# Optimization experiments

Hardware: AMD Instinct MI355X
Metric: run time of the kernel (lower is better)

## Reference

```python
import jax, jax.numpy as jnp
import numpy as np

L, B, T, C, H, V, CTX = 4, 2, 1024, 1024, 16, 50257, 2048
D = C // H
EPS = 1e-5
NEG_SLOPE = 0.01


def layer_norm(x, w, b):
    mu = jnp.mean(x, axis=-1, keepdims=True)
    var = jnp.mean(jnp.square(x - mu), axis=-1, keepdims=True)
    return (x - mu) * jax.lax.rsqrt(var + EPS) * w + b


def setup_inputs() -> dict:
    key = jax.random.key(0)
    ks = jax.random.split(key, 8)
    s = 0.02  # init std as in _init_weights
    return {
        "idx": jax.random.randint(ks[0], (B, T), 0, V),
        "wte": jax.random.normal(ks[1], (V, C), jnp.float32) * s,
        "wpe": jax.random.normal(ks[2], (CTX, C), jnp.float32) * s,
        "ln1_w": jnp.ones((L, C), jnp.float32),
        "ln1_b": jnp.zeros((L, C), jnp.float32),
        "attn_w": jax.random.normal(ks[3], (L, C, 3 * C), jnp.float32) * s,
        "attn_b": jnp.zeros((L, 3 * C), jnp.float32),
        "proj_w": jax.random.normal(ks[4], (L, C, C), jnp.float32) * s,
        "proj_b": jnp.zeros((L, C), jnp.float32),
        "ln2_w": jnp.ones((L, C), jnp.float32),
        "ln2_b": jnp.zeros((L, C), jnp.float32),
        "fc_w": jax.random.normal(ks[5], (L, C, 4 * C), jnp.float32) * s,
        "fc_b": jnp.zeros((L, 4 * C), jnp.float32),
        "fcproj_w": jax.random.normal(ks[6], (L, 4 * C, C), jnp.float32) * s,
        "fcproj_b": jnp.zeros((L, C), jnp.float32),
        "lnf_w": jnp.ones((C,), jnp.float32),
        "lnf_b": jnp.zeros((C,), jnp.float32),
    }


def reference(idx, wte, wpe, ln1_w, ln1_b, attn_w, attn_b, proj_w, proj_b,
              ln2_w, ln2_b, fc_w, fc_b, fcproj_w, fcproj_b, lnf_w, lnf_b):
    t = idx.shape[1]
    x = wte[idx] + wpe[:t]  # [B,T,C]; dropout=0 => identity
    causal = jnp.tril(jnp.ones((t, t), bool))  # [T,T]
    scale = 1.0 / np.sqrt(D)
    for l in range(L):
        # --- causal self-attention ---
        h = layer_norm(x, ln1_w[l], ln1_b[l])
        qkv = h @ attn_w[l] + attn_b[l]  # [B,T,3C]
        q, k, v = jnp.split(qkv, 3, axis=-1)
        q = q.reshape(B, t, H, D)
        k = k.reshape(B, t, H, D)
        v = v.reshape(B, t, H, D)
        att = jnp.einsum('bthd,bshd->bhts', q, k) * scale  # [B,H,T,T]
        att = jnp.where(causal, att, -jnp.inf)
        att = jax.nn.softmax(att, axis=-1)
        y = jnp.einsum('bhts,bshd->bthd', att, v).reshape(B, t, C)
        x = x + y @ proj_w[l] + proj_b[l]
        # --- MLP ---
        h = layer_norm(x, ln2_w[l], ln2_b[l])
        h = h @ fc_w[l] + fc_b[l]
        h = jnp.where(h >= 0, h, NEG_SLOPE * h)  # LeakyReLU(0.01)
        x = x + h @ fcproj_w[l] + fcproj_b[l]
    x = layer_norm(x, lnf_w, lnf_b)
    # targets=None path: lm_head on last position only, tied weight = wte
    logits = x[:, -1:, :] @ wte.T  # [B,1,V]
    return logits
```

## Files before the change

### kernel.cpp

```cpp
#include <hip/hip_runtime.h>
#include <hip/hip_bf16.h>


#define TT 1024
#define CC 1024
#define NHEAD 16
#define DHEAD 64
#define NBATCH 2
#define VOCAB 50257

typedef __attribute__((ext_vector_type(8))) short bf16x8;
typedef __attribute__((ext_vector_type(4))) float f32x4;

#define GPTR(p) (const __attribute__((address_space(1))) void*)(p)
#define LPTR(p) (__attribute__((address_space(3))) void*)(p)

__device__ __forceinline__ unsigned short f2bf(float f) {
  union { float f; unsigned u; } v; v.f = f;
  unsigned r = v.u + 0x7fffu + ((v.u >> 16) & 1u);
  return (unsigned short)(r >> 16);
}
__device__ __forceinline__ float bf2f(unsigned short u) {
  union { unsigned u; float f; } v; v.u = ((unsigned)u) << 16;
  return v.f;
}

__device__ __forceinline__ f32x4 mfma_bf16(bf16x8 a, bf16x8 b, f32x4 c) {
  return __builtin_amdgcn_mfma_f32_16x16x32_bf16(a, b, c, 0, 0, 0);
}

__device__ __forceinline__ unsigned pk2(float lo, float hi) {
  return (unsigned)f2bf(lo) | ((unsigned)f2bf(hi) << 16);
}

__global__ __launch_bounds__(256) void embedln_k(const int* __restrict__ idx,
    const float* __restrict__ wte, const float* __restrict__ wpe,
    const float* __restrict__ lw, const float* __restrict__ lb,
    float* __restrict__ x, unsigned short* __restrict__ h)
{
  __shared__ float rs[4], rss[4];
  const int row = blockIdx.x;
  const int t = row & (TT - 1);
  const int tok = idx[row];
  const int tid = threadIdx.x, wave = tid >> 6, lane = tid & 63;
  float4 va = ((const float4*)(wte + (size_t)tok * CC))[tid];
  float4 vp = ((const float4*)(wpe + (size_t)t * CC))[tid];
  float4 v = make_float4(va.x + vp.x, va.y + vp.y, va.z + vp.z, va.w + vp.w);
  ((float4*)(x + (size_t)row * CC))[tid] = v;
  float s  = v.x + v.y + v.z + v.w;
  float ss = v.x*v.x + v.y*v.y + v.z*v.z + v.w*v.w;
#pragma unroll
  for (int off = 1; off < 64; off <<= 1) {
    s  += __shfl_xor(s, off, 64);
    ss += __shfl_xor(ss, off, 64);
  }
  if (lane == 0) { rs[wave] = s; rss[wave] = ss; }
  __syncthreads();
  s  = rs[0] + rs[1] + rs[2] + rs[3];
  ss = rss[0] + rss[1] + rss[2] + rss[3];
  float mu = s * (1.f / CC);
  float var = ss * (1.f / CC) - mu * mu;
  float rstd = rsqrtf(var + 1e-5f);
  float4 wv = ((const float4*)lw)[tid];
  float4 bv = ((const float4*)lb)[tid];
  float o0 = (v.x - mu) * rstd * wv.x + bv.x;
  float o1 = (v.y - mu) * rstd * wv.y + bv.y;
  float o2 = (v.z - mu) * rstd * wv.z + bv.z;
  float o3 = (v.w - mu) * rstd * wv.w + bv.w;
  ((uint2*)(h + (size_t)row * CC))[tid] = make_uint2(pk2(o0, o1), pk2(o2, o3));
}

__global__ __launch_bounds__(256) void redln_k(float* __restrict__ x,
    const float* __restrict__ P, const float* __restrict__ bias,
    const float* __restrict__ lw, const float* __restrict__ lb,
    unsigned short* __restrict__ out, int splits)
{
  int row = blockIdx.x * 4 + (threadIdx.x >> 6);
  int lane = threadIdx.x & 63;
  const int c0 = lane * 16;
  float* xw = x + (size_t)row * CC + c0;
  float4 v[4];
#pragma unroll
  for (int i = 0; i < 4; ++i) v[i] = *(const float4*)(xw + i * 4);
  {
    const float4* b4 = (const float4*)(bias + c0);
#pragma unroll
    for (int i = 0; i < 4; ++i) {
      float4 bv = b4[i];
      v[i].x += bv.x; v[i].y += bv.y; v[i].z += bv.z; v[i].w += bv.w;
    }
  }
  for (int sp = 0; sp < splits; ++sp) {
    const float4* p4 = (const float4*)(P + ((size_t)sp * 2048 + row) * CC + c0);
#pragma unroll
    for (int i = 0; i < 4; ++i) {
      float4 pv = p4[i];
      v[i].x += pv.x; v[i].y += pv.y; v[i].z += pv.z; v[i].w += pv.w;
    }
  }
  float s = 0.f, ss = 0.f;
#pragma unroll
  for (int i = 0; i < 4; ++i) {
    *(float4*)(xw + i * 4) = v[i];
    s  += v[i].x + v[i].y + v[i].z + v[i].w;
    ss += v[i].x*v[i].x + v[i].y*v[i].y + v[i].z*v[i].z + v[i].w*v[i].w;
  }
#pragma unroll
  for (int off = 1; off < 64; off <<= 1) {
    s  += __shfl_xor(s, off, 64);
    ss += __shfl_xor(ss, off, 64);
  }
  float mu = s * (1.f / CC);
  float var = ss * (1.f / CC) - mu * mu;
  float rstd = rsqrtf(var + 1e-5f);
  const float* wr = lw + c0;
  const float* br = lb + c0;
  unsigned q[8];
#pragma unroll
  for (int i = 0; i < 4; ++i) {
    float4 wv = *(const float4*)(wr + i * 4);
    float4 bv = *(const float4*)(br + i * 4);
    float o0 = (v[i].x - mu) * rstd * wv.x + bv.x;
    float o1 = (v[i].y - mu) * rstd * wv.y + bv.y;
    float o2 = (v[i].z - mu) * rstd * wv.z + bv.z;
    float o3 = (v[i].w - mu) * rstd * wv.w + bv.w;
    q[i*2+0] = pk2(o0, o1);
    q[i*2+1] = pk2(o2, o3);
  }
  uint4* op = (uint4*)(out + (size_t)row * CC + c0);
  op[0] = make_uint4(q[0], q[1], q[2], q[3]);
  op[1] = make_uint4(q[4], q[5], q[6], q[7]);
}

__global__ __launch_bounds__(256) void wconv_all_k(
    const float* __restrict__ attn_w, unsigned short* __restrict__ wt_attn,
    const float* __restrict__ proj_w, unsigned short* __restrict__ wt_proj,
    const float* __restrict__ fc_w,   unsigned short* __restrict__ wt_fc,
    const float* __restrict__ fcp_w,  unsigned short* __restrict__ wt_fcp)
{
  int b = blockIdx.x;
  const float* W; unsigned short* Wt; int K, N, kx, ny;
  if (b < 3072) {
    int layer = b / 768, tI = b % 768;
    K = 1024; N = 3072;
    W = attn_w + (size_t)layer * K * N; Wt = wt_attn + (size_t)layer * K * N;
    kx = tI % 16; ny = tI / 16;
  } else if (b < 3840) {
    b -= 3072; int layer = b / 256, tI = b % 256;
    K = 1024; N = 1024;
    W = proj_w + (size_t)layer * K * N; Wt = wt_proj + (size_t)layer * K * N;
    kx = tI % 16; ny = tI / 16;
  } else if (b < 6912) {
    b -= 3840; int layer = b / 1024, tI = b % 1024;
    K = 1024; N = 4096;
    W = fc_w + (size_t)layer * K * N; Wt = wt_fc + (size_t)layer * K * N;
    kx = tI % 16; ny = tI / 16;
  } else {
    b -= 6912; int layer = b / 1024, tI = b % 1024;
    K = 4096; N = 1024;
    W = fcp_w + (size_t)layer * K * N; Wt = wt_fcp + (size_t)layer * K * N;
    kx = tI % 64; ny = tI / 64;
  }
  __shared__ float tile[64][65];
  const int k0 = kx << 6, n0 = ny << 6;
  const int t = threadIdx.x;
  {
    const int r = t >> 4, c4 = t & 15;
#pragma unroll
    for (int p = 0; p < 4; ++p) {
      int kr = r + (p << 4);
      float4 v = *(const float4*)(W + (size_t)(k0 + kr) * N + n0 + (c4 << 2));
      tile[kr][(c4 << 2) + 0] = v.x;
      tile[kr][(c4 << 2) + 1] = v.y;
      tile[kr][(c4 << 2) + 2] = v.z;
      tile[kr][(c4 << 2) + 3] = v.w;
    }
  }
  __syncthreads();
  {
    const int n = t >> 2, kq = t & 3;
    bf16x8 o0, o1;
#pragma unroll
    for (int e = 0; e < 8; ++e) o0[e] = (short)f2bf(tile[(kq << 4) + e][n]);
#pragma unroll
    for (int e = 0; e < 8; ++e) o1[e] = (short)f2bf(tile[(kq << 4) + 8 + e][n]);
    unsigned short* dst = Wt + (size_t)(n0 + n) * K + k0 + (kq << 4);
    *(bf16x8*)dst = o0;
    *(bf16x8*)(dst + 8) = o1;
  }
}

#define MODE_QKV  0
#define MODE_PART 1
#define MODE_FC   2

template<int MODE>
__global__ __launch_bounds__(256) void gemm_k(
    const unsigned short* __restrict__ A,
    const unsigned short* __restrict__ Wt,
    const float* __restrict__ bias,
    float* __restrict__ pbuf,
    unsigned short* __restrict__ obf,
    unsigned short* __restrict__ q_o,
    unsigned short* __restrict__ k_o,
    unsigned short* __restrict__ v_o,
    int M, int N, int K, int kchunk, int ncol0)
{
  __shared__ alignas(16) unsigned short Asm[2][128 * 64];
  __shared__ alignas(16) unsigned short Bsm[2][128 * 64];
  const int tid  = threadIdx.x;
  const int wave = tid >> 6, lane = tid & 63;
  const int lg = lane >> 4, ll = lane & 15;
  const int nTM = M >> 7, nTN = N >> 7;
  int bid = blockIdx.x;
  const int mt = bid % nTM; bid /= nTM;
  const int nt = bid % nTN;
  const int s  = bid / nTN;
  const int m0 = mt << 7, n0 = nt << 7;
  const int kb = s * kchunk;
  const int nIter = kchunk >> 6;
  const int wm = (wave >> 1) << 6, wn = (wave & 1) << 6;
  f32x4 acc[4][4] = {};

#define STAGE(BUF, K0)                                                        \
  {                                                                           \
    _Pragma("unroll")                                                         \
    for (int c = 0; c < 4; ++c) {                                             \
      const int seg = (wave << 2) + c;                                        \
      const int g = (seg << 6) + lane;                                        \
      const int row = g >> 3, kq = g & 7;                                     \
      const unsigned short* asrc = A  + (size_t)(m0 + row) * K + (K0) + (kq << 3); \
      const unsigned short* bsrc = Wt + (size_t)(n0 + row) * K + (K0) + (kq << 3); \
      __builtin_amdgcn_global_load_lds(GPTR(asrc), LPTR(&Asm[BUF][seg << 9]), 16, 0, 0); \
      __builtin_amdgcn_global_load_lds(GPTR(bsrc), LPTR(&Bsm[BUF][seg << 9]), 16, 0, 0); \
    }                                                                         \
  }

  STAGE(0, kb);
  if (nIter > 1) STAGE(1, kb + 64);

  for (int t = 0; t < nIter; ++t) {
    const int cur = t & 1;
    if (t + 1 < nIter) { asm volatile("s_waitcnt vmcnt(8)" ::: "memory"); }
    else               { asm volatile("s_waitcnt vmcnt(0)" ::: "memory"); }
    __builtin_amdgcn_sched_barrier(0);
    __builtin_amdgcn_s_barrier();

    const unsigned short* As = &Asm[cur][0];
    const unsigned short* Bs = &Bsm[cur][0];
#pragma unroll
    for (int kk = 0; kk < 2; ++kk) {
      bf16x8 af[4], bfr[4];
#pragma unroll
      for (int i = 0; i < 4; ++i)
        af[i] = *(const bf16x8*)(As + ((wm + i * 16 + ll) << 6) + (kk << 5) + (lg << 3));
#pragma unroll
      for (int j = 0; j < 4; ++j)
        bfr[j] = *(const bf16x8*)(Bs + ((wn + j * 16 + ll) << 6) + (kk << 5) + (lg << 3));
#pragma unroll
      for (int i = 0; i < 4; ++i)
#pragma unroll
        for (int j = 0; j < 4; ++j)
          acc[i][j] = mfma_bf16(af[i], bfr[j], acc[i][j]);
    }
    __builtin_amdgcn_sched_barrier(0);
    __builtin_amdgcn_s_barrier();
    if (t + 2 < nIter) STAGE(cur, kb + ((t + 2) << 6));
  }
#undef STAGE

#pragma unroll
  for (int j = 0; j < 4; ++j) {
    int gc = n0 + wn + j * 16 + ll;
    int gcol = ncol0 + gc;
    float bv = (MODE == MODE_PART) ? 0.f : bias[gcol];
#pragma unroll
    for (int i = 0; i < 4; ++i) {
      int gr0 = m0 + wm + i * 16 + (lg << 2);
#pragma unroll
      for (int r = 0; r < 4; ++r) {
        int grow = gr0 + r;
        float val = acc[i][j][r] + bv;
        if (MODE == MODE_QKV) {
          int which = gcol >> 10;
          int head = (gcol >> 6) & 15;
          int d = gcol & 63;
          int bb = grow >> 10, tt2 = grow & (TT - 1);
          unsigned short* dst = (which == 0) ? q_o : (which == 1) ? k_o : v_o;
          dst[(((size_t)((bb << 4) + head)) << 16) + ((size_t)tt2 << 6) + d] = f2bf(val);
        } else if (MODE == MODE_FC) {
          val = (val >= 0.f) ? val : 0.01f * val;
          obf[(size_t)grow * N + gc] = f2bf(val);
        } else {
          pbuf[((size_t)s * M + grow) * N + gc] = val;
        }
      }
    }
  }
}

__global__ __launch_bounds__(256) void attn_k(
    const unsigned short* __restrict__ Qb,
    const unsigned short* __restrict__ Kb,
    const unsigned short* __restrict__ Vb,
    unsigned short* __restrict__ ybuf)
{
  __shared__ alignas(16) unsigned short Ksm[64][72];
  __shared__ alignas(16) unsigned short Vtsm[64][64];
  __shared__ alignas(16) unsigned short Psm[4][16][72];
  const int tid = threadIdx.x;
  const int wave = tid >> 6, lane = tid & 63;
  const int lg = lane >> 4, ll = lane & 15;
  const int qt = blockIdx.x & 15, bh = blockIdx.x >> 4;
  const int b = bh >> 4, h = bh & 15;
  const size_t base = (size_t)bh << 16;
  const int q0 = qt << 6;
  const float SC = 0.125f * 1.44269504f;

  const int qrow = q0 + wave * 16 + ll;
  bf16x8 aq0 = *(const bf16x8*)(Qb + base + ((size_t)qrow << 6) + (lg << 3));
  bf16x8 aq1 = *(const bf16x8*)(Qb + base + ((size_t)qrow << 6) + 32 + (lg << 3));

  f32x4 accy[4] = {};
  float m_run[4], l_run[4];
#pragma unroll
  for (int r = 0; r < 4; ++r) { m_run[r] = -1e30f; l_run[r] = 0.f; }

  const int sk_row = tid >> 3, sk_cq = tid & 7;
  const int sv_d = tid & 63, sv_kq = tid >> 6;
  const int qg0 = q0 + wave * 16 + (lg << 2);

  for (int kb = 0; kb <= qt; ++kb) {
    const int kbase = kb << 6;
#pragma unroll
    for (int p = 0; p < 2; ++p) {
      int r = sk_row + (p << 5);
      bf16x8 kv = *(const bf16x8*)(Kb + base + ((size_t)(kbase + r) << 6) + (sk_cq << 3));
      *(bf16x8*)&Ksm[r][sk_cq << 3] = kv;
    }
#pragma unroll
    for (int p = 0; p < 2; ++p) {
      int kq8 = sv_kq + (p << 2);
      bf16x8 wv;
#pragma unroll
      for (int e = 0; e < 8; ++e)
        wv[e] = (short)Vb[base + ((size_t)(kbase + (kq8 << 3) + e) << 6) + sv_d];
      int u = kq8 ^ (sv_d & 7);
      *(bf16x8*)&Vtsm[sv_d][u << 3] = wv;
    }
    __syncthreads();

    float p_[4][4];
    float rmax[4] = {-1e30f, -1e30f, -1e30f, -1e30f};
#pragma unroll
    for (int kk = 0; kk < 4; ++kk) {
      f32x4 z = {};
      bf16x8 bk0 = *(const bf16x8*)&Ksm[kk * 16 + ll][lg << 3];
      bf16x8 bk1 = *(const bf16x8*)&Ksm[kk * 16 + ll][32 + (lg << 3)];
      z = mfma_bf16(aq0, bk0, z);
      z = mfma_bf16(aq1, bk1, z);
      int key = kbase + kk * 16 + ll;
#pragma unroll
      for (int r = 0; r < 4; ++r) {
        float v = z[r] * SC;
        v = (key > qg0 + r) ? -1e30f : v;
        p_[kk][r] = v;
        rmax[r] = fmaxf(rmax[r], v);
      }
    }
#pragma unroll
    for (int off = 1; off < 16; off <<= 1)
#pragma unroll
      for (int r = 0; r < 4; ++r)
        rmax[r] = fmaxf(rmax[r], __shfl_xor(rmax[r], off, 64));

    float alpha[4], rsum[4];
#pragma unroll
    for (int r = 0; r < 4; ++r) {
      float mn = fmaxf(m_run[r], rmax[r]);
      alpha[r] = exp2f(m_run[r] - mn);
      m_run[r] = mn;
      rsum[r] = 0.f;
    }
#pragma unroll
    for (int kk = 0; kk < 4; ++kk)
#pragma unroll
      for (int r = 0; r < 4; ++r) {
        float e = exp2f(p_[kk][r] - m_run[r]);
        p_[kk][r] = e;
        rsum[r] += e;
      }
#pragma unroll
    for (int off = 1; off < 16; off <<= 1)
#pragma unroll
      for (int r = 0; r < 4; ++r)
        rsum[r] += __shfl_xor(rsum[r], off, 64);
#pragma unroll
    for (int r = 0; r < 4; ++r)
      l_run[r] = l_run[r] * alpha[r] + rsum[r];
#pragma unroll
    for (int df = 0; df < 4; ++df)
#pragma unroll
      for (int r = 0; r < 4; ++r)
        accy[df][r] *= alpha[r];

#pragma unroll
    for (int kk = 0; kk < 4; ++kk)
#pragma unroll
      for (int r = 0; r < 4; ++r)
        Psm[wave][(lg << 2) + r][kk * 16 + ll] = f2bf(p_[kk][r]);
    bf16x8 pa0 = *(const bf16x8*)&Psm[wave][ll][lg << 3];
    bf16x8 pa1 = *(const bf16x8*)&Psm[wave][ll][32 + (lg << 3)];

#pragma unroll
    for (int df = 0; df < 4; ++df) {
      int d = df * 16 + ll;
      int u0 = lg ^ (d & 7);
      int u1 = (4 + lg) ^ (d & 7);
      bf16x8 bv0 = *(const bf16x8*)&Vtsm[d][u0 << 3];
      bf16x8 bv1 = *(const bf16x8*)&Vtsm[d][u1 << 3];
      accy[df] = mfma_bf16(pa0, bv0, accy[df]);
      accy[df] = mfma_bf16(pa1, bv1, accy[df]);
    }
    __syncthreads();
  }

#pragma unroll
  for (int df = 0; df < 4; ++df)
#pragma unroll
    for (int r = 0; r < 4; ++r) {
      int qr = qg0 + r;
      float y = accy[df][r] / l_run[r];
      ybuf[(((size_t)((b << 10) + qr)) << 10) + (h << 6) + df * 16 + ll] = f2bf(y);
    }
}


__global__ __launch_bounds__(256) void qlast_k(
    const unsigned short* __restrict__ hbuf,
    const float* __restrict__ Wq,
    float* __restrict__ qpart)
{
  __shared__ float xs[2][128];
  const int tid = threadIdx.x, ks = blockIdx.y;
  {
    const int b = tid >> 7, j = tid & 127;
    xs[b][j] = bf2f(hbuf[((size_t)(b * TT + TT - 1)) * CC + ks * 128 + j]);
  }
  __syncthreads();
  const int n = blockIdx.x * 256 + tid;
  float a0 = 0.f, a1 = 0.f;
  const float* wp = Wq + (size_t)(ks * 128) * 3072 + n;
  for (int k = 0; k < 128; k += 8)
#pragma unroll
    for (int u = 0; u < 8; ++u) {
      float w = wp[(size_t)(k + u) * 3072];
      a0 += xs[0][k + u] * w;
      a1 += xs[1][k + u] * w;
    }
  qpart[(size_t)(ks * 2 + 0) * 1024 + n] = a0;
  qpart[(size_t)(ks * 2 + 1) * 1024 + n] = a1;
}

__global__ __launch_bounds__(256) void attnlast2_k(
    const float* __restrict__ qpart, const float* __restrict__ bq,
    const unsigned short* __restrict__ Kb,
    const unsigned short* __restrict__ Vb,
    float* __restrict__ y_last)
{
  __shared__ float qs[64];
  __shared__ float wm[4], wl[4], wacc[4][64];
  const int tid = threadIdx.x;
  const int wave = tid >> 6, lane = tid & 63;
  const int bh = blockIdx.x;
  const int b = bh >> 4, h = bh & 15;
  const size_t base = (size_t)bh << 16;
  if (tid < 64) {
    const int col = h * 64 + tid;
    float q = bq[col];
#pragma unroll
    for (int ks = 0; ks < 8; ++ks)
      q += qpart[(size_t)(ks * 2 + b) * 1024 + col];
    qs[tid] = q;
  }
  __syncthreads();

  float m_w = -1e30f, l_w = 0.f, acc = 0.f;
  for (int ks = 0; ks < 4; ++ks) {
    const int key = ks * 256 + wave * 64 + lane;
    float s = 0.f;
    const unsigned short* kp = Kb + base + ((size_t)key << 6);
#pragma unroll
    for (int o = 0; o < 8; ++o) {
      bf16x8 kv = *(const bf16x8*)(kp + (o << 3));
#pragma unroll
      for (int e = 0; e < 8; ++e)
        s += qs[(o << 3) + e] * bf2f((unsigned short)kv[e]);
    }
    s *= 0.125f;
    float m = s;
#pragma unroll
    for (int off = 1; off < 64; off <<= 1)
      m = fmaxf(m, __shfl_xor(m, off, 64));
    float mn = fmaxf(m_w, m);
    float alpha = __expf(m_w - mn);
    m_w = mn;
    float p = __expf(s - mn);
    float ps = p;
#pragma unroll
    for (int off = 1; off < 64; off <<= 1)
      ps += __shfl_xor(ps, off, 64);
    l_w = l_w * alpha + ps;
    float a2 = 0.f;
    const unsigned short* vp = Vb + base + ((size_t)(ks * 256 + wave * 64) << 6);
    for (int j = 0; j < 64; ++j) {
      float pj = __shfl(p, j, 64);
      a2 += pj * bf2f(vp[((size_t)j << 6) + lane]);
    }
    acc = acc * alpha + a2;
  }
  if (lane == 0) { wm[wave] = m_w; wl[wave] = l_w; }
  wacc[wave][lane] = acc;
  __syncthreads();
  if (wave == 0) {
    float m0 = fmaxf(fmaxf(wm[0], wm[1]), fmaxf(wm[2], wm[3]));
    float lt = 0.f, at = 0.f;
#pragma unroll
    for (int sI = 0; sI < 4; ++sI) {
      float f = __expf(wm[sI] - m0);
      lt += wl[sI] * f;
      at += wacc[sI][lane] * f;
    }
    y_last[b * CC + h * 64 + lane] = at / lt;
  }
}

__global__ __launch_bounds__(256) void projpart_k(
    const float* __restrict__ ylast,
    const float* __restrict__ W,
    float* __restrict__ ppart)
{
  __shared__ float xs[2][128];
  const int tid = threadIdx.x, ks = blockIdx.y;
  {
    const int b = tid >> 7, j = tid & 127;
    xs[b][j] = ylast[b * 1024 + ks * 128 + j];
  }
  __syncthreads();
  const int n = blockIdx.x * 256 + tid;
  float a0 = 0.f, a1 = 0.f;
  const float* wp = W + (size_t)(ks * 128) * 1024 + n;
  for (int k = 0; k < 128; k += 8)
#pragma unroll
    for (int u = 0; u < 8; ++u) {
      float w = wp[(size_t)(k + u) * 1024];
      a0 += xs[0][k + u] * w;
      a1 += xs[1][k + u] * w;
    }
  ppart[(size_t)(ks * 2 + 0) * 1024 + n] = a0;
  ppart[(size_t)(ks * 2 + 1) * 1024 + n] = a1;
}

__global__ __launch_bounds__(256) void fclast_k(
    const float* __restrict__ x, const float* __restrict__ ppart,
    const float* __restrict__ pbias,
    const float* __restrict__ lw, const float* __restrict__ lb,
    const float* __restrict__ W,
    float* __restrict__ fcpart)
{
  __shared__ float xs[2][1024];
  const int tid = threadIdx.x;
  const int wave = tid >> 6, lane = tid & 63;
  if (wave < 2) {
    const int c0 = lane * 16;
    const float* xr = x + ((size_t)(wave * TT + TT - 1)) * CC + c0;
    float4 v[4];
    float s = 0.f, ss = 0.f;
#pragma unroll
    for (int i = 0; i < 4; ++i) {
      v[i] = *(const float4*)(xr + i * 4);
      float4 bv = *(const float4*)(pbias + c0 + i * 4);
      v[i].x += bv.x; v[i].y += bv.y; v[i].z += bv.z; v[i].w += bv.w;
    }
#pragma unroll
    for (int sp = 0; sp < 8; ++sp) {
      const float* pp = ppart + (size_t)(sp * 2 + wave) * 1024 + c0;
#pragma unroll
      for (int i = 0; i < 4; ++i) {
        float4 pv = *(const float4*)(pp + i * 4);
        v[i].x += pv.x; v[i].y += pv.y; v[i].z += pv.z; v[i].w += pv.w;
      }
    }
#pragma unroll
    for (int i = 0; i < 4; ++i) {
      s  += v[i].x + v[i].y + v[i].z + v[i].w;
      ss += v[i].x*v[i].x + v[i].y*v[i].y + v[i].z*v[i].z + v[i].w*v[i].w;
    }
#pragma unroll
    for (int off = 1; off < 64; off <<= 1) {
      s  += __shfl_xor(s, off, 64);
      ss += __shfl_xor(ss, off, 64);
    }
    float mu = s * (1.f / CC);
    float var = ss * (1.f / CC) - mu * mu;
    float rstd = rsqrtf(var + 1e-5f);
#pragma unroll
    for (int i = 0; i < 4; ++i) {
      float4 wv = *(const float4*)(lw + c0 + i * 4);
      float4 bv = *(const float4*)(lb + c0 + i * 4);
      xs[wave][c0 + i * 4 + 0] = (v[i].x - mu) * rstd * wv.x + bv.x;
      xs[wave][c0 + i * 4 + 1] = (v[i].y - mu) * rstd * wv.y + bv.y;
      xs[wave][c0 + i * 4 + 2] = (v[i].z - mu) * rstd * wv.z + bv.z;
      xs[wave][c0 + i * 4 + 3] = (v[i].w - mu) * rstd * wv.w + bv.w;
    }
  }
  __syncthreads();
  const int ks = blockIdx.y;
  const int n = blockIdx.x * 256 + tid;
  float a0 = 0.f, a1 = 0.f;
  const float* wp = W + (size_t)(ks * 128) * 4096 + n;
  for (int k = 0; k < 128; k += 8)
#pragma unroll
    for (int u = 0; u < 8; ++u) {
      float w = wp[(size_t)(k + u) * 4096];
      a0 += xs[0][ks * 128 + k + u] * w;
      a1 += xs[1][ks * 128 + k + u] * w;
    }
  fcpart[(size_t)(ks * 2 + 0) * 4096 + n] = a0;
  fcpart[(size_t)(ks * 2 + 1) * 4096 + n] = a1;
}

__global__ __launch_bounds__(256) void fcprojpart_k(
    const float* __restrict__ fcpart, const float* __restrict__ fcbias,
    const float* __restrict__ W,
    float* __restrict__ fppart)
{
  __shared__ float hs[2][512];
  const int tid = threadIdx.x, ks = blockIdx.y;
#pragma unroll
  for (int i = 0; i < 4; ++i) {
    const int e = tid + 256 * i;
    const int b = e >> 9, j = e & 511;
    const int c = ks * 512 + j;
    float v = fcbias[c];
#pragma unroll
    for (int sp = 0; sp < 8; ++sp)
      v += fcpart[(size_t)(sp * 2 + b) * 4096 + c];
    hs[b][j] = (v >= 0.f) ? v : 0.01f * v;
  }
  __syncthreads();
  const int n = blockIdx.x * 256 + tid;
  float a0 = 0.f, a1 = 0.f;
  const float* wp = W + (size_t)(ks * 512) * 1024 + n;
  for (int k = 0; k < 512; k += 8)
#pragma unroll
    for (int u = 0; u < 8; ++u) {
      float w = wp[(size_t)(k + u) * 1024];
      a0 += hs[0][k + u] * w;
      a1 += hs[1][k + u] * w;
    }
  fppart[(size_t)(ks * 2 + 0) * 1024 + n] = a0;
  fppart[(size_t)(ks * 2 + 1) * 1024 + n] = a1;
}

__global__ void lnfmerge_k(const float* __restrict__ x,
    const float* __restrict__ ppart, const float* __restrict__ pbias,
    const float* __restrict__ fppart, const float* __restrict__ fpbias,
    const float* __restrict__ lw, const float* __restrict__ lb,
    float* __restrict__ xf)
{
  const int row = blockIdx.x;
  const int lane = threadIdx.x;
  const int c0 = lane * 16;
  const float* xr = x + ((size_t)(row * TT + TT - 1)) * CC + c0;
  float4 v[4];
  float s = 0.f, ss = 0.f;
#pragma unroll
  for (int i = 0; i < 4; ++i) {
    v[i] = *(const float4*)(xr + i * 4);
    float4 b1 = *(const float4*)(pbias + c0 + i * 4);
    float4 b2 = *(const float4*)(fpbias + c0 + i * 4);
    v[i].x += b1.x + b2.x; v[i].y += b1.y + b2.y;
    v[i].z += b1.z + b2.z; v[i].w += b1.w + b2.w;
  }
#pragma unroll
  for (int sp = 0; sp < 8; ++sp) {
    const float* p1 = ppart + (size_t)(sp * 2 + row) * 1024 + c0;
    const float* p2 = fppart + (size_t)(sp * 2 + row) * 1024 + c0;
#pragma unroll
    for (int i = 0; i < 4; ++i) {
      float4 a = *(const float4*)(p1 + i * 4);
      float4 b = *(const float4*)(p2 + i * 4);
      v[i].x += a.x + b.x; v[i].y += a.y + b.y;
      v[i].z += a.z + b.z; v[i].w += a.w + b.w;
    }
  }
#pragma unroll
  for (int i = 0; i < 4; ++i) {
    s  += v[i].x + v[i].y + v[i].z + v[i].w;
    ss += v[i].x*v[i].x + v[i].y*v[i].y + v[i].z*v[i].z + v[i].w*v[i].w;
  }
#pragma unroll
  for (int off = 1; off < 64; off <<= 1) {
    s  += __shfl_xor(s, off, 64);
    ss += __shfl_xor(ss, off, 64);
  }
  float mu = s * (1.f / CC);
  float var = ss * (1.f / CC) - mu * mu;
  float rstd = rsqrtf(var + 1e-5f);
  float* op = xf + (size_t)row * CC + c0;
#pragma unroll
  for (int i = 0; i < 4; ++i) {
    float4 wv = *(const float4*)(lw + c0 + i * 4);
    float4 bv = *(const float4*)(lb + c0 + i * 4);
    float4 o;
    o.x = (v[i].x - mu) * rstd * wv.x + bv.x;
    o.y = (v[i].y - mu) * rstd * wv.y + bv.y;
    o.z = (v[i].z - mu) * rstd * wv.z + bv.z;
    o.w = (v[i].w - mu) * rstd * wv.w + bv.w;
    *(float4*)(op + i * 4) = o;
  }
}

__global__ __launch_bounds__(256) void head_k(const float* __restrict__ xf,
    const float* __restrict__ wte, float* __restrict__ out)
{
  int v = (blockIdx.x << 2) + (threadIdx.x >> 6);
  if (v >= VOCAB) return;
  int lane = threadIdx.x & 63;
  const float4* wr = (const float4*)(wte + (size_t)v * CC);
  const float4* x0 = (const float4*)xf;
  const float4* x1 = (const float4*)(xf + CC);
  float a0 = 0.f, a1 = 0.f;
#pragma unroll
  for (int i = 0; i < 4; ++i) {
    float4 wv = wr[lane + i * 64];
    float4 p0 = x0[lane + i * 64];
    float4 p1 = x1[lane + i * 64];
    a0 += wv.x * p0.x + wv.y * p0.y + wv.z * p0.z + wv.w * p0.w;
    a1 += wv.x * p1.x + wv.y * p1.y + wv.z * p1.z + wv.w * p1.w;
  }
#pragma unroll
  for (int off = 1; off < 64; off <<= 1) {
    a0 += __shfl_xor(a0, off, 64);
    a1 += __shfl_xor(a1, off, 64);
  }
  if (lane == 0) {
    out[v] = a0;
    out[VOCAB + v] = a1;
  }
}

extern "C" void kernel_launch(void* const* d_in, const int* in_sizes, int n_in,
                              void* d_out, int out_size, void* d_ws, size_t ws_size,
                              hipStream_t stream)
{
  const int*   idx      = (const int*)d_in[0];
  const float* wte      = (const float*)d_in[1];
  const float* wpe      = (const float*)d_in[2];
  const float* ln1_w    = (const float*)d_in[3];
  const float* ln1_b    = (const float*)d_in[4];
  const float* attn_w   = (const float*)d_in[5];
  const float* attn_b   = (const float*)d_in[6];
  const float* proj_w   = (const float*)d_in[7];
  const float* proj_b   = (const float*)d_in[8];
  const float* ln2_w    = (const float*)d_in[9];
  const float* ln2_b    = (const float*)d_in[10];
  const float* fc_w     = (const float*)d_in[11];
  const float* fc_b     = (const float*)d_in[12];
  const float* fcproj_w = (const float*)d_in[13];
  const float* fcproj_b = (const float*)d_in[14];
  const float* lnf_w    = (const float*)d_in[15];
  const float* lnf_b    = (const float*)d_in[16];
  float* out = (float*)d_out;

  const size_t MB = 1u << 20;
  char* ws = (char*)d_ws;
  float*          x   = (float*)ws;
  unsigned short* h   = (unsigned short*)(ws + 8*MB);
  unsigned short* qb  = (unsigned short*)(ws + 12*MB);
  unsigned short* kb_ = (unsigned short*)(ws + 16*MB);
  unsigned short* vb  = (unsigned short*)(ws + 20*MB);
  unsigned short* yb  = (unsigned short*)(ws + 24*MB);
  unsigned short* hf  = (unsigned short*)(ws + 28*MB);
  char* sm = ws + 44*MB;
  float* xf     = (float*)(sm + 0);
  float* ylast  = (float*)(sm + 16*1024);
  float* qpart  = (float*)(sm + 64*1024);
  float* ppart  = (float*)(sm + 128*1024);
  float* fppart = (float*)(sm + 192*1024);
  float* fcpart = (float*)(sm + 256*1024);
  unsigned short* wt_attn   = (unsigned short*)(ws + 46*MB);
  unsigned short* wt_proj   = (unsigned short*)(ws + 70*MB);
  unsigned short* wt_fc     = (unsigned short*)(ws + 76*MB);
  unsigned short* wt_fcproj = (unsigned short*)(ws + 100*MB);
  float*          Ppart     = (float*)(ws + 124*MB);

  embedln_k<<<NBATCH * TT, 256, 0, stream>>>(idx, wte, wpe, ln1_w, ln1_b, x, h);

  wconv_all_k<<<9984, 256, 0, stream>>>(attn_w, wt_attn, proj_w, wt_proj,
                                        fc_w, wt_fc, fcproj_w, wt_fcproj);

  for (int l = 0; l < 3; ++l) {
    gemm_k<MODE_QKV><<<16 * 24, 256, 0, stream>>>(h,
        wt_attn + (size_t)l * 3072 * 1024, attn_b + (size_t)l * 3 * CC,
        nullptr, nullptr, qb, kb_, vb, 2048, 3072, 1024, 1024, 0);
    attn_k<<<NBATCH * NHEAD * 16, 256, 0, stream>>>(qb, kb_, vb, yb);
    gemm_k<MODE_PART><<<16 * 8 * 4, 256, 0, stream>>>(yb,
        wt_proj + (size_t)l * 1024 * 1024, nullptr,
        Ppart, nullptr, nullptr, nullptr, nullptr, 2048, 1024, 1024, 256, 0);
    redln_k<<<512, 256, 0, stream>>>(x, Ppart, proj_b + l * CC,
        ln2_w + l * CC, ln2_b + l * CC, h, 4);
    gemm_k<MODE_FC><<<16 * 32, 256, 0, stream>>>(h,
        wt_fc + (size_t)l * 1024 * 4096, fc_b + (size_t)l * 4 * CC,
        nullptr, hf, nullptr, nullptr, nullptr, 2048, 4096, 1024, 1024, 0);
    gemm_k<MODE_PART><<<16 * 8 * 4, 256, 0, stream>>>(hf,
        wt_fcproj + (size_t)l * 4096 * 1024, nullptr,
        Ppart, nullptr, nullptr, nullptr, nullptr, 2048, 1024, 4096, 1024, 0);
    redln_k<<<512, 256, 0, stream>>>(x, Ppart, fcproj_b + l * CC,
        ln1_w + (l + 1) * CC, ln1_b + (l + 1) * CC, h, 4);
  }

  {
    const int l = 3;
    gemm_k<MODE_QKV><<<16 * 16, 256, 0, stream>>>(h,
        wt_attn + (size_t)l * 3072 * 1024 + (size_t)1024 * 1024,
        attn_b + (size_t)l * 3 * CC,
        nullptr, nullptr, qb, kb_, vb, 2048, 2048, 1024, 1024, 1024);
    qlast_k<<<dim3(4, 8), 256, 0, stream>>>(h,
        attn_w + (size_t)l * CC * 3 * CC, qpart);
    attnlast2_k<<<32, 256, 0, stream>>>(qpart, attn_b + (size_t)l * 3 * CC,
        kb_, vb, ylast);
    projpart_k<<<dim3(4, 8), 256, 0, stream>>>(ylast,
        proj_w + (size_t)l * CC * CC, ppart);
    fclast_k<<<dim3(16, 8), 256, 0, stream>>>(x, ppart, proj_b + l * CC,
        ln2_w + l * CC, ln2_b + l * CC,
        fc_w + (size_t)l * CC * 4 * CC, fcpart);
    fcprojpart_k<<<dim3(4, 8), 256, 0, stream>>>(fcpart,
        fc_b + (size_t)l * 4 * CC, fcproj_w + (size_t)l * 4 * CC * CC, fppart);
    lnfmerge_k<<<2, 64, 0, stream>>>(x, ppart, proj_b + l * CC,
        fppart, fcproj_b + l * CC, lnf_w, lnf_b, xf);
  }

  head_k<<<(VOCAB + 3) / 4, 256, 0, stream>>>(xf, wte, out);
}
```

Baseline: 673.0 us.

## Store V transposed, bf16 split-K partials, widen final LN merge kernel

The QKV GEMM now writes V in a [d][t] transposed layout, so attention kernels load V with vectorized 16-byte reads instead of strided scalar gathers. Split-K partial sums for the projection GEMMs are stored as bf16 instead of fp32, which halves partial-buffer traffic but adds rounding error in the residual accumulation. The final layernorm merge kernel is widened from 64 to 256 threads per row.

```diff
diff --git a/kernel.cpp b/kernel.cpp
--- a/kernel.cpp
+++ b/kernel.cpp
@@ -71,7 +71,7 @@
 }
 
 __global__ __launch_bounds__(256) void redln_k(float* __restrict__ x,
-    const float* __restrict__ P, const float* __restrict__ bias,
+    const unsigned short* __restrict__ P, const float* __restrict__ bias,
     const float* __restrict__ lw, const float* __restrict__ lb,
     unsigned short* __restrict__ out, int splits)
 {
@@ -91,12 +91,17 @@
     }
   }
   for (int sp = 0; sp < splits; ++sp) {
-    const float4* p4 = (const float4*)(P + ((size_t)sp * 2048 + row) * CC + c0);
-#pragma unroll
-    for (int i = 0; i < 4; ++i) {
-      float4 pv = p4[i];
-      v[i].x += pv.x; v[i].y += pv.y; v[i].z += pv.z; v[i].w += pv.w;
-    }
+    const unsigned short* pp = P + ((size_t)sp * 2048 + row) * CC + c0;
+    bf16x8 pa = *(const bf16x8*)pp;
+    bf16x8 pb = *(const bf16x8*)(pp + 8);
+    v[0].x += bf2f((unsigned short)pa[0]); v[0].y += bf2f((unsigned short)pa[1]);
+    v[0].z += bf2f((unsigned short)pa[2]); v[0].w += bf2f((unsigned short)pa[3]);
+    v[1].x += bf2f((unsigned short)pa[4]); v[1].y += bf2f((unsigned short)pa[5]);
+    v[1].z += bf2f((unsigned short)pa[6]); v[1].w += bf2f((unsigned short)pa[7]);
+    v[2].x += bf2f((unsigned short)pb[0]); v[2].y += bf2f((unsigned short)pb[1]);
+    v[2].z += bf2f((unsigned short)pb[2]); v[2].w += bf2f((unsigned short)pb[3]);
+    v[3].x += bf2f((unsigned short)pb[4]); v[3].y += bf2f((unsigned short)pb[5]);
+    v[3].z += bf2f((unsigned short)pb[6]); v[3].w += bf2f((unsigned short)pb[7]);
   }
   float s = 0.f, ss = 0.f;
 #pragma unroll
@@ -199,7 +204,6 @@
     const unsigned short* __restrict__ A,
     const unsigned short* __restrict__ Wt,
     const float* __restrict__ bias,
-    float* __restrict__ pbuf,
     unsigned short* __restrict__ obf,
     unsigned short* __restrict__ q_o,
     unsigned short* __restrict__ k_o,
@@ -286,13 +290,15 @@
           int head = (gcol >> 6) & 15;
           int d = gcol & 63;
           int bb = grow >> 10, tt2 = grow & (TT - 1);
-          unsigned short* dst = (which == 0) ? q_o : (which == 1) ? k_o : v_o;
-          dst[(((size_t)((bb << 4) + head)) << 16) + ((size_t)tt2 << 6) + d] = f2bf(val);
+          size_t bhb = ((size_t)((bb << 4) + head)) << 16;
+          if (which == 2)      v_o[bhb + ((size_t)d << 10) + tt2] = f2bf(val);
+          else if (which == 1) k_o[bhb + ((size_t)tt2 << 6) + d] = f2bf(val);
+          else                 q_o[bhb + ((size_t)tt2 << 6) + d] = f2bf(val);
         } else if (MODE == MODE_FC) {
           val = (val >= 0.f) ? val : 0.01f * val;
           obf[(size_t)grow * N + gc] = f2bf(val);
         } else {
-          pbuf[((size_t)s * M + grow) * N + gc] = val;
+          obf[((size_t)s * M + grow) * N + gc] = f2bf(val);
         }
       }
     }
@@ -341,10 +347,7 @@
 #pragma unroll
     for (int p = 0; p < 2; ++p) {
       int kq8 = sv_kq + (p << 2);
-      bf16x8 wv;
-#pragma unroll
-      for (int e = 0; e < 8; ++e)
-        wv[e] = (short)Vb[base + ((size_t)(kbase + (kq8 << 3) + e) << 6) + sv_d];
+      bf16x8 wv = *(const bf16x8*)(Vb + base + ((size_t)sv_d << 10) + kbase + (kq8 << 3));
       int u = kq8 ^ (sv_d & 7);
       *(bf16x8*)&Vtsm[sv_d][u << 3] = wv;
     }
@@ -512,10 +515,15 @@
       ps += __shfl_xor(ps, off, 64);
     l_w = l_w * alpha + ps;
     float a2 = 0.f;
-    const unsigned short* vp = Vb + base + ((size_t)(ks * 256 + wave * 64) << 6);
-    for (int j = 0; j < 64; ++j) {
-      float pj = __shfl(p, j, 64);
-      a2 += pj * bf2f(vp[((size_t)j << 6) + lane]);
+    const unsigned short* vp = Vb + base + ((size_t)lane << 10) + ks * 256 + wave * 64;
+#pragma unroll
+    for (int j8 = 0; j8 < 8; ++j8) {
+      bf16x8 vv = *(const bf16x8*)(vp + (j8 << 3));
+#pragma unroll
+      for (int e = 0; e < 8; ++e) {
+        float pj = __shfl(p, (j8 << 3) + e, 64);
+        a2 += pj * bf2f((unsigned short)vv[e]);
+      }
     }
     acc = acc * alpha + a2;
   }
@@ -663,63 +671,53 @@
   fppart[(size_t)(ks * 2 + 1) * 1024 + n] = a1;
 }
 
-__global__ void lnfmerge_k(const float* __restrict__ x,
+__global__ __launch_bounds__(256) void lnfmerge_k(const float* __restrict__ x,
     const float* __restrict__ ppart, const float* __restrict__ pbias,
     const float* __restrict__ fppart, const float* __restrict__ fpbias,
     const float* __restrict__ lw, const float* __restrict__ lb,
     float* __restrict__ xf)
 {
+  __shared__ float rs[4], rss[4];
   const int row = blockIdx.x;
-  const int lane = threadIdx.x;
-  const int c0 = lane * 16;
-  const float* xr = x + ((size_t)(row * TT + TT - 1)) * CC + c0;
-  float4 v[4];
-  float s = 0.f, ss = 0.f;
-#pragma unroll
-  for (int i = 0; i < 4; ++i) {
-    v[i] = *(const float4*)(xr + i * 4);
-    float4 b1 = *(const float4*)(pbias + c0 + i * 4);
-    float4 b2 = *(const float4*)(fpbias + c0 + i * 4);
-    v[i].x += b1.x + b2.x; v[i].y += b1.y + b2.y;
-    v[i].z += b1.z + b2.z; v[i].w += b1.w + b2.w;
+  const int tid = threadIdx.x;
+  const int wave = tid >> 6, lane = tid & 63;
+  const int c0 = tid * 4;
+  float4 v = *(const float4*)(x + ((size_t)(row * TT + TT - 1)) * CC + c0);
+  {
+    float4 b1 = *(const float4*)(pbias + c0);
+    float4 b2 = *(const float4*)(fpbias + c0);
+    v.x += b1.x + b2.x; v.y += b1.y + b2.y;
+    v.z += b1.z + b2.z; v.w += b1.w + b2.w;
   }
 #pragma unroll
   for (int sp = 0; sp < 8; ++sp) {
-    const float* p1 = ppart + (size_t)(sp * 2 + row) * 1024 + c0;
-    const float* p2 = fppart + (size_t)(sp * 2 + row) * 1024 + c0;
-#pragma unroll
-    for (int i = 0; i < 4; ++i) {
-      float4 a = *(const float4*)(p1 + i * 4);
-      float4 b = *(const float4*)(p2 + i * 4);
-      v[i].x += a.x + b.x; v[i].y += a.y + b.y;
-      v[i].z += a.z + b.z; v[i].w += a.w + b.w;
-    }
-  }
-#pragma unroll
-  for (int i = 0; i < 4; ++i) {
-    s  += v[i].x + v[i].y + v[i].z + v[i].w;
-    ss += v[i].x*v[i].x + v[i].y*v[i].y + v[i].z*v[i].z + v[i].w*v[i].w;
-  }
+    float4 a = *(const float4*)(ppart + (size_t)(sp * 2 + row) * 1024 + c0);
+    float4 b = *(const float4*)(fppart + (size_t)(sp * 2 + row) * 1024 + c0);
+    v.x += a.x + b.x; v.y += a.y + b.y;
+    v.z += a.z + b.z; v.w += a.w + b.w;
+  }
+  float s  = v.x + v.y + v.z + v.w;
+  float ss = v.x*v.x + v.y*v.y + v.z*v.z + v.w*v.w;
 #pragma unroll
   for (int off = 1; off < 64; off <<= 1) {
     s  += __shfl_xor(s, off, 64);
     ss += __shfl_xor(ss, off, 64);
   }
+  if (lane == 0) { rs[wave] = s; rss[wave] = ss; }
+  __syncthreads();
+  s  = rs[0] + rs[1] + rs[2] + rs[3];
+  ss = rss[0] + rss[1] + rss[2] + rss[3];
   float mu = s * (1.f / CC);
   float var = ss * (1.f / CC) - mu * mu;
   float rstd = rsqrtf(var + 1e-5f);
-  float* op = xf + (size_t)row * CC + c0;
-#pragma unroll
-  for (int i = 0; i < 4; ++i) {
-    float4 wv = *(const float4*)(lw + c0 + i * 4);
-    float4 bv = *(const float4*)(lb + c0 + i * 4);
-    float4 o;
-    o.x = (v[i].x - mu) * rstd * wv.x + bv.x;
-    o.y = (v[i].y - mu) * rstd * wv.y + bv.y;
-    o.z = (v[i].z - mu) * rstd * wv.z + bv.z;
-    o.w = (v[i].w - mu) * rstd * wv.w + bv.w;
-    *(float4*)(op + i * 4) = o;
-  }
+  float4 wv = *(const float4*)(lw + c0);
+  float4 bv = *(const float4*)(lb + c0);
+  float4 o;
+  o.x = (v.x - mu) * rstd * wv.x + bv.x;
+  o.y = (v.y - mu) * rstd * wv.y + bv.y;
+  o.z = (v.z - mu) * rstd * wv.z + bv.z;
+  o.w = (v.w - mu) * rstd * wv.w + bv.w;
+  *(float4*)(xf + (size_t)row * CC + c0) = o;
 }
 
 __global__ __launch_bounds__(256) void head_k(const float* __restrict__ xf,
@@ -794,7 +792,7 @@
   unsigned short* wt_proj   = (unsigned short*)(ws + 70*MB);
   unsigned short* wt_fc     = (unsigned short*)(ws + 76*MB);
   unsigned short* wt_fcproj = (unsigned short*)(ws + 100*MB);
-  float*          Ppart     = (float*)(ws + 124*MB);
+  unsigned short* Ppart     = (unsigned short*)(ws + 124*MB);
 
   embedln_k<<<NBATCH * TT, 256, 0, stream>>>(idx, wte, wpe, ln1_w, ln1_b, x, h);
 
@@ -804,19 +802,19 @@
   for (int l = 0; l < 3; ++l) {
     gemm_k<MODE_QKV><<<16 * 24, 256, 0, stream>>>(h,
         wt_attn + (size_t)l * 3072 * 1024, attn_b + (size_t)l * 3 * CC,
-        nullptr, nullptr, qb, kb_, vb, 2048, 3072, 1024, 1024, 0);
+        nullptr, qb, kb_, vb, 2048, 3072, 1024, 1024, 0);
     attn_k<<<NBATCH * NHEAD * 16, 256, 0, stream>>>(qb, kb_, vb, yb);
     gemm_k<MODE_PART><<<16 * 8 * 4, 256, 0, stream>>>(yb,
         wt_proj + (size_t)l * 1024 * 1024, nullptr,
-        Ppart, nullptr, nullptr, nullptr, nullptr, 2048, 1024, 1024, 256, 0);
+        Ppart, nullptr, nullptr, nullptr, 2048, 1024, 1024, 256, 0);
     redln_k<<<512, 256, 0, stream>>>(x, Ppart, proj_b + l * CC,
         ln2_w + l * CC, ln2_b + l * CC, h, 4);
     gemm_k<MODE_FC><<<16 * 32, 256, 0, stream>>>(h,
         wt_fc + (size_t)l * 1024 * 4096, fc_b + (size_t)l * 4 * CC,
-        nullptr, hf, nullptr, nullptr, nullptr, 2048, 4096, 1024, 1024, 0);
+        hf, nullptr, nullptr, nullptr, 2048, 4096, 1024, 1024, 0);
     gemm_k<MODE_PART><<<16 * 8 * 4, 256, 0, stream>>>(hf,
         wt_fcproj + (size_t)l * 4096 * 1024, nullptr,
-        Ppart, nullptr, nullptr, nullptr, nullptr, 2048, 1024, 4096, 1024, 0);
+        Ppart, nullptr, nullptr, nullptr, 2048, 1024, 4096, 1024, 0);
     redln_k<<<512, 256, 0, stream>>>(x, Ppart, fcproj_b + l * CC,
         ln1_w + (l + 1) * CC, ln1_b + (l + 1) * CC, h, 4);
   }
@@ -826,7 +824,7 @@
     gemm_k<MODE_QKV><<<16 * 16, 256, 0, stream>>>(h,
         wt_attn + (size_t)l * 3072 * 1024 + (size_t)1024 * 1024,
         attn_b + (size_t)l * 3 * CC,
-        nullptr, nullptr, qb, kb_, vb, 2048, 2048, 1024, 1024, 1024);
+        nullptr, qb, kb_, vb, 2048, 2048, 1024, 1024, 1024);
     qlast_k<<<dim3(4, 8), 256, 0, stream>>>(h,
         attn_w + (size_t)l * CC * 3 * CC, qpart);
     attnlast2_k<<<32, 256, 0, stream>>>(qpart, attn_b + (size_t)l * 3 * CC,
@@ -838,7 +836,7 @@
         fc_w + (size_t)l * CC * 4 * CC, fcpart);
     fcprojpart_k<<<dim3(4, 8), 256, 0, stream>>>(fcpart,
         fc_b + (size_t)l * 4 * CC, fcproj_w + (size_t)l * 4 * CC * CC, fppart);
-    lnfmerge_k<<<2, 64, 0, stream>>>(x, ppart, proj_b + l * CC,
+    lnfmerge_k<<<2, 256, 0, stream>>>(x, ppart, proj_b + l * CC,
         fppart, fcproj_b + l * CC, lnf_w, lnf_b, xf);
   }
 
```

After: 668.1 us. Within noise of the previous version (-0.7%).
